# Kernel tuning notes

Measured on AMD Instinct MI355X. Metric: run time of the kernel, lower is better.

## Reference

```python
import jax, jax.numpy as jnp
import numpy as np

VOCAB = 50000
E = 256      # text_embed_dim
K = 512      # num_kernels
KS = 9       # kernel_size
L = 8192     # num labels
B, T = 8, 2048
PAD = KS // 2


def setup_inputs() -> dict:
    key = jax.random.key(0)
    ks = jax.random.split(key, 9)
    ids = jax.random.randint(ks[0], (B, T), 0, VOCAB)
    mask = jnp.ones((B, T), dtype=jnp.int32)  # unused by forward, kept for signature parity
    target = (jax.random.uniform(ks[1], (B, L)) < 0.01).astype(jnp.float32)
    embed_w = jax.random.normal(ks[2], (VOCAB, E), jnp.float32) * 0.02
    conv_w = jax.random.normal(ks[3], (K, E, KS), jnp.float32) * (1.0 / np.sqrt(E * KS))
    conv_b = jnp.zeros((K,), jnp.float32)
    U_w = jax.random.normal(ks[4], (L, K), jnp.float32) * (1.0 / np.sqrt(K))
    final_w = jax.random.normal(ks[5], (L, K), jnp.float32) * (1.0 / np.sqrt(K))
    final_b = jnp.zeros((L,), jnp.float32)
    return {"ids": ids, "mask": mask, "G": 0, "target": target,
            "embed_w": embed_w, "conv_w": conv_w, "conv_b": conv_b,
            "U_w": U_w, "final_w": final_w, "final_b": final_b}


def _forward(ids, embed_w, conv_w, conv_b, U_w, final_w, final_b):
    # embed + (dropout=identity in eval) -> [B, E, T]
    x = embed_w[ids].transpose(0, 2, 1)
    # same-padded Conv1d, then ReLU -> text_feats [B, T, K]
    y = jax.lax.conv_general_dilated(x, conv_w, (1,), [(PAD, PAD)],
                                     dimension_numbers=("NCH", "OIH", "NCH"))
    feats = jax.nn.relu(y + conv_b[None, :, None]).transpose(0, 2, 1)
    # label-wise attention: alpha = softmax(U.weight @ feats^T, dim=2) -> [B, L, T]
    scores = jnp.einsum("lk,btk->blt", U_w, feats)
    alpha = jax.nn.softmax(scores, axis=2)
    # attended features per label -> [B, L, K]
    attn = jnp.einsum("blt,btk->blk", alpha, feats)
    # label-wise dot with final.weight + bias -> logits [B, L]
    yhat = jnp.einsum("blk,lk->bl", attn, final_w) + final_b
    return yhat


def _bce_with_logits(yhat, target):
    # mean over all elements, numerically stable
    return jnp.mean(jnp.maximum(yhat, 0) - yhat * target + jnp.log1p(jnp.exp(-jnp.abs(yhat))))


def reference(ids, mask, G, target, embed_w, conv_w, conv_b, U_w, final_w, final_b):
    yhat = _forward(ids, embed_w, conv_w, conv_b, U_w, final_w, final_b)
    loss = _bce_with_logits(yhat, target)
    return yhat, loss
```

## Files before the change

kernel.cpp:

```cpp
#include <hip/hip_runtime.h>
#include <hip/hip_bf16.h>
#include <cstdint>

#define B_ 8
#define T_ 2048
#define E_ 256
#define K_ 512
#define KS_ 9
#define L_ 8192
#define PAD_ 4
#define TP_ (T_ + 2 * PAD_)
#define KK_ (E_ * KS_)

#define FEAT_SCALE 64.0f
#define W_SCALE 16.0f
#define INV_SS 9.765625e-4f

typedef __bf16 bf16x8 __attribute__((ext_vector_type(8)));
typedef float f32x4 __attribute__((ext_vector_type(4)));
typedef float f32x16 __attribute__((ext_vector_type(16)));
typedef int i32x4 __attribute__((ext_vector_type(4)));
typedef int i32x8 __attribute__((ext_vector_type(8)));

__device__ __forceinline__ unsigned short f2bf(float f) {
  union { float f; unsigned int u; } a; a.f = f;
  unsigned int r = (a.u + 0x7FFFu + ((a.u >> 16) & 1u)) >> 16;
  return (unsigned short)r;
}

__device__ __forceinline__ unsigned char f2fp8(float v) {
  return (unsigned char)(__builtin_amdgcn_cvt_pk_fp8_f32(v, v, 0, false) & 0xFF);
}

__device__ __forceinline__ unsigned int pk4_fp8(float a, float b, float c, float d) {
  int v = __builtin_amdgcn_cvt_pk_fp8_f32(a, b, 0, false);
  v = __builtin_amdgcn_cvt_pk_fp8_f32(c, d, v, true);
  return (unsigned int)v;
}

__device__ __forceinline__ void gld_lds16(const void* g, void* l) {
  __builtin_amdgcn_global_load_lds(
      (const __attribute__((address_space(1))) unsigned int*)g,
      (__attribute__((address_space(3))) unsigned int*)l, 16, 0, 0);
}

__device__ __forceinline__ f32x4 mfma_bf16(bf16x8 a, bf16x8 b, f32x4 c) {
  return __builtin_amdgcn_mfma_f32_16x16x32_bf16(a, b, c, 0, 0, 0);
}

__device__ __forceinline__ f32x16 mfma_sc64(i32x8 a, i32x8 b, f32x16 c) {
  return __builtin_amdgcn_mfma_scale_f32_32x32x64_f8f6f4(a, b, c, 0, 0, 0, 127, 0, 127);
}

__device__ __forceinline__ int swz_off(int k, int row) {
  int ku = k >> 4;
  int slot = ((ku & 7) ^ (row & 7)) | (ku & 24);
  return slot * 16 + (k & 15);
}

__global__ __launch_bounds__(256) void k_embed(const int* __restrict__ ids,
                                               const float* __restrict__ emb,
                                               unsigned short* __restrict__ xpad) {
  int gid = blockIdx.x * 256 + threadIdx.x;
  int row = gid >> 6;
  int e4 = (gid & 63) << 2;
  int b = row / TP_;
  int tp = row - b * TP_;
  float4 v = make_float4(0.f, 0.f, 0.f, 0.f);
  if (tp >= PAD_ && tp < T_ + PAD_) {
    int id = ids[b * T_ + tp - PAD_];
    v = *(const float4*)(emb + (size_t)id * E_ + e4);
  }
  ushort4 o;
  o.x = f2bf(v.x); o.y = f2bf(v.y); o.z = f2bf(v.z); o.w = f2bf(v.w);
  *(ushort4*)(xpad + (size_t)row * E_ + e4) = o;
}

__global__ __launch_bounds__(256) void k_wt(const float* __restrict__ conv_w,
                                            unsigned short* __restrict__ wt) {
  int kk = blockIdx.x * 256 + threadIdx.x;
  int k = blockIdx.y;
  int j = kk >> 8, e = kk & 255;
  wt[(size_t)k * KK_ + kk] = f2bf(conv_w[(k * E_ + e) * KS_ + j]);
}

__global__ __launch_bounds__(256) void k_cast(const float* __restrict__ U_w,
                                              const float* __restrict__ F_w,
                                              unsigned char* __restrict__ u8,
                                              unsigned char* __restrict__ f8) {
  int gid = blockIdx.x * 256 + threadIdx.x;
  const float* src = blockIdx.y ? F_w : U_w;
  unsigned char* dst = blockIdx.y ? f8 : u8;
  int l = gid >> 6;
  int k0 = (gid & 63) << 3;
  const float* s = src + (size_t)l * K_ + k0;
  float4 v0 = *(const float4*)(s);
  float4 v1 = *(const float4*)(s + 4);
  uint2 o;
  o.x = pk4_fp8(v0.x * W_SCALE, v0.y * W_SCALE, v0.z * W_SCALE, v0.w * W_SCALE);
  o.y = pk4_fp8(v1.x * W_SCALE, v1.y * W_SCALE, v1.z * W_SCALE, v1.w * W_SCALE);
  *(uint2*)(dst + (size_t)l * K_ + swz_off(k0, l)) = o;
}

__global__ __launch_bounds__(512, 4) void k_conv(const unsigned short* __restrict__ xpad,
                                                 const unsigned short* __restrict__ wt,
                                                 const float* __restrict__ conv_b,
                                                 unsigned char* __restrict__ feats) {
  __shared__ char At[2][16384];
  __shared__ char Bt[2][16384];
  const int tid = threadIdx.x;
  const int lane = tid & 63;
  const int q = lane >> 4, c = lane & 15;
  const int w = tid >> 6;
  const int wi = w >> 1, wj = w & 1;
  const int b = blockIdx.z;
  const int t0 = blockIdx.y * 128;
  const int n0 = blockIdx.x * 128;

  const char* xb = (const char*)(xpad + (size_t)b * TP_ * E_);
  const char* wb = (const char*)wt;

  const char* asrc[2]; const char* bsrc[2]; int ldso[2];
#pragma unroll
  for (int rnd = 0; rnd < 2; ++rnd) {
    int u = rnd * 512 + tid;
    int r = u >> 3;
    int j = (u & 7) ^ (r & 7);
    asrc[rnd] = xb + (size_t)(t0 + r) * 512 + j * 16;
    bsrc[rnd] = wb + (size_t)(n0 + r) * (KK_ * 2) + j * 16;
    ldso[rnd] = u * 16;
  }

  int offA[2][2], offB[4][2];
#pragma unroll
  for (int li = 0; li < 2; ++li) {
    int r = wi * 32 + li * 16 + c;
#pragma unroll
    for (int h = 0; h < 2; ++h) offA[li][h] = r * 128 + (((4 * h + q) ^ (r & 7)) << 4);
  }
#pragma unroll
  for (int ti = 0; ti < 4; ++ti) {
    int r = wj * 64 + ti * 16 + c;
#pragma unroll
    for (int h = 0; h < 2; ++h) offB[ti][h] = r * 128 + (((4 * h + q) ^ (r & 7)) << 4);
  }

  f32x4 acc[2][4];
  f32x4 zero = {0.f, 0.f, 0.f, 0.f};
#pragma unroll
  for (int i = 0; i < 2; ++i)
#pragma unroll
    for (int j = 0; j < 4; ++j) acc[i][j] = zero;

#pragma unroll
  for (int rnd = 0; rnd < 2; ++rnd) {
    gld_lds16(asrc[rnd], At[0] + ldso[rnd]);
    gld_lds16(bsrc[rnd], Bt[0] + ldso[rnd]);
  }

  for (int it = 0; it < 36; ++it) {
    const int bsel = it & 1;
    __syncthreads();
    if (it != 35) {
      const int kkc = (it + 1) * 64;
      const int aofs = (kkc >> 8) * 512 + (kkc & 255) * 2;
      const int bofs = kkc * 2;
#pragma unroll
      for (int rnd = 0; rnd < 2; ++rnd) {
        gld_lds16(asrc[rnd] + aofs, At[bsel ^ 1] + ldso[rnd]);
        gld_lds16(bsrc[rnd] + bofs, Bt[bsel ^ 1] + ldso[rnd]);
      }
    }
    const char* aB = At[bsel];
    const char* bB = Bt[bsel];
#pragma unroll
    for (int h = 0; h < 2; ++h) {
      bf16x8 afr[2], bfr[4];
#pragma unroll
      for (int li = 0; li < 2; ++li) afr[li] = *(const bf16x8*)(aB + offA[li][h]);
#pragma unroll
      for (int ti = 0; ti < 4; ++ti) bfr[ti] = *(const bf16x8*)(bB + offB[ti][h]);
#pragma unroll
      for (int ti = 0; ti < 4; ++ti)
#pragma unroll
        for (int li = 0; li < 2; ++li)
          acc[li][ti] = mfma_bf16(afr[li], bfr[ti], acc[li][ti]);
    }
  }

#pragma unroll
  for (int ti = 0; ti < 4; ++ti) {
    int k = n0 + wj * 64 + ti * 16 + c;
    float bias = conv_b[k];
#pragma unroll
    for (int li = 0; li < 2; ++li) {
      int tb = t0 + wi * 32 + li * 16 + q * 4;
#pragma unroll
      for (int rr = 0; rr < 4; ++rr) {
        float v = fmaxf(acc[li][ti][rr] + bias, 0.f) * FEAT_SCALE;
        int t = tb + rr;
        feats[(size_t)(b * T_ + t) * K_ + swz_off(k, t)] = f2fp8(v);
      }
    }
  }
}

__global__ __launch_bounds__(512, 2) void k_attn(const unsigned char* __restrict__ feats,
                                                 const unsigned char* __restrict__ u8,
                                                 const unsigned char* __restrict__ f8,
                                                 const float* __restrict__ final_b,
                                                 float* __restrict__ out) {
  __shared__ __align__(16) char smem[131072];
  __shared__ float red[512];
  const int tid = threadIdx.x;
  const int lane = tid & 63;
  const int q2 = lane >> 5, c32 = lane & 31;
  const int w = tid >> 6;
  const int wi = w >> 1;
  const int wj = w & 1;
  const int b = blockIdx.y;
  const int l0 = blockIdx.x * 128;

  const unsigned char* fb = feats + (size_t)b * T_ * K_;

  char* Us = smem;
  char* Ws = smem + 65536;
#pragma unroll
  for (int rr = 0; rr < 8; ++rr) {
    gld_lds16(u8 + (size_t)l0 * K_ + rr * 8192 + tid * 16, Us + rr * 8192 + tid * 16);
    gld_lds16(f8 + (size_t)l0 * K_ + rr * 8192 + tid * 16, Ws + rr * 8192 + tid * 16);
  }
  __syncthreads();

  const int arow = wi * 32 + c32;
  const int ab = arow * 512;
  const int a7 = arow & 7;
  i32x8 uf[8], wf[8];
#pragma unroll
  for (int s = 0; s < 8; ++s) {
    int u0 = s * 4 + q2 * 2;
    int o0 = ab + ((((u0 & 7) ^ a7) | (u0 & 24)) << 4);
    i32x4 ul = *(const i32x4*)(Us + o0);
    i32x4 uh = *(const i32x4*)(Us + (o0 ^ 16));
    i32x4 wl = *(const i32x4*)(Ws + o0);
    i32x4 wh = *(const i32x4*)(Ws + (o0 ^ 16));
    uf[s] = __builtin_shufflevector(ul, uh, 0, 1, 2, 3, 4, 5, 6, 7);
    wf[s] = __builtin_shufflevector(wl, wh, 0, 1, 2, 3, 4, 5, 6, 7);
  }
  __syncthreads();

  char* const Fs0 = smem;
  char* const Fs1 = smem + 32768;
  const unsigned char* fsrc = fb + tid * 16;
#pragma unroll
  for (int rr = 0; rr < 4; ++rr)
    gld_lds16(fsrc + rr * 8192, Fs0 + tid * 16 + rr * 8192);

  const int brow = wj * 32 + c32;
  const int bb = brow * 512;
  const int b7 = brow & 7;
  int foff[8];
#pragma unroll
  for (int s = 0; s < 8; ++s) {
    int u0 = s * 4 + q2 * 2;
    foff[s] = bb + ((((u0 & 7) ^ b7) | (u0 & 24)) << 4);
  }

  f32x16 accS, accV;
  float num[16], den[16];
#pragma unroll
  for (int r = 0; r < 16; ++r) { accS[r] = 0.f; accV[r] = 0.f; num[r] = 0.f; den[r] = 0.f; }

  for (int tc = 0; tc < 32; ++tc) {
    const int bsel = tc & 1;
    char* const cur = bsel ? Fs1 : Fs0;
    char* const nxt = bsel ? Fs0 : Fs1;
    __syncthreads();
    if (tc != 31) {
      const unsigned char* nsrc = fsrc + (tc + 1) * 32768;
#pragma unroll
      for (int rr = 0; rr < 4; ++rr)
        gld_lds16(nsrc + rr * 8192, nxt + tid * 16 + rr * 8192);
    }
#pragma unroll
    for (int s = 0; s < 8; ++s) {
      i32x4 flo = *(const i32x4*)(cur + foff[s]);
      i32x4 fhi = *(const i32x4*)(cur + (foff[s] ^ 16));
      i32x8 fa = __builtin_shufflevector(flo, fhi, 0, 1, 2, 3, 4, 5, 6, 7);
      accS = mfma_sc64(uf[s], fa, accS);
      accV = mfma_sc64(wf[s], fa, accV);
    }
#pragma unroll
    for (int r = 0; r < 16; ++r) {
      float p = __expf(accS[r] * INV_SS);
      den[r] += p;
      num[r] += p * accV[r];
      accS[r] = 0.f;
      accV[r] = 0.f;
    }
  }

#pragma unroll
  for (int r = 0; r < 16; ++r) {
#pragma unroll
    for (int m = 1; m < 32; m <<= 1) {
      num[r] += __shfl_xor(num[r], m, 64);
      den[r] += __shfl_xor(den[r], m, 64);
    }
  }
  if (c32 == 0) {
#pragma unroll
    for (int r = 0; r < 16; ++r) {
      int ll = wi * 32 + (r & 3) + 8 * (r >> 2) + 4 * q2;
      red[wj * 256 + ll] = num[r];
      red[wj * 256 + 128 + ll] = den[r];
    }
  }
  __syncthreads();
  if (tid < 128) {
    int l = l0 + tid;
    float n = red[tid] + red[256 + tid];
    float d = red[128 + tid] + red[384 + tid];
    out[(size_t)b * L_ + l] = (n * INV_SS) / d + final_b[l];
  }
}

__global__ __launch_bounds__(256) void k_loss(const float* __restrict__ yhat,
                                              const float* __restrict__ target,
                                              float* __restrict__ loss) {
  int gid = blockIdx.x * 256 + threadIdx.x;
  float s = 0.f;
  for (int i = gid; i < B_ * L_; i += 64 * 256) {
    float y = yhat[i], t = target[i];
    s += fmaxf(y, 0.f) - y * t + log1pf(__expf(-fabsf(y)));
  }
#pragma unroll
  for (int m = 1; m < 64; m <<= 1) s += __shfl_xor(s, m, 64);
  if ((threadIdx.x & 63) == 0) atomicAdd(loss, s * (1.0f / (B_ * L_)));
}

extern "C" void kernel_launch(void* const* d_in, const int* in_sizes, int n_in,
                              void* d_out, int out_size, void* d_ws, size_t ws_size,
                              hipStream_t stream) {
  const int* ids = (const int*)d_in[0];
  const float* target = (const float*)d_in[3];
  const float* emb = (const float*)d_in[4];
  const float* conv_w = (const float*)d_in[5];
  const float* conv_b = (const float*)d_in[6];
  const float* U_w = (const float*)d_in[7];
  const float* F_w = (const float*)d_in[8];
  const float* final_b = (const float*)d_in[9];
  float* out = (float*)d_out;

  char* ws = (char*)d_ws;
  unsigned short* xpad = (unsigned short*)ws;
  size_t off = (size_t)B_ * TP_ * E_ * 2;
  unsigned short* wt = (unsigned short*)(ws + off);
  off += (size_t)K_ * KK_ * 2;
  unsigned char* u8 = (unsigned char*)(ws + off);
  off += (size_t)L_ * K_;
  unsigned char* f8 = (unsigned char*)(ws + off);
  off += (size_t)L_ * K_;
  unsigned char* feats = (unsigned char*)(ws + off);
  off += (size_t)B_ * T_ * K_;
  if (ws_size < off) return;

  k_embed<<<dim3((B_ * TP_ * 64) / 256), 256, 0, stream>>>(ids, emb, xpad);
  k_wt<<<dim3(KK_ / 256, K_), 256, 0, stream>>>(conv_w, wt);
  k_cast<<<dim3((L_ * K_ / 8) / 256, 2), 256, 0, stream>>>(U_w, F_w, u8, f8);
  k_conv<<<dim3(K_ / 128, T_ / 128, B_), 512, 0, stream>>>(xpad, wt, conv_b, feats);
  k_attn<<<dim3(L_ / 128, B_), 512, 0, stream>>>(feats, u8, f8, final_b, out);
  hipMemsetAsync(out + B_ * L_, 0, sizeof(float), stream);
  k_loss<<<dim3(64), 256, 0, stream>>>(out, target, out + B_ * L_);
}
```

Baseline: 288.0 us.

## Store feats and fp8 weights in k-chunk-major tiles, use exp2 in softmax

Replaces the XOR-swizzled row-major layout of the fp8 features and weight matrices with a blocked layout: 16-byte k-chunks are stored contiguously across rows within each 64-row (feats) or 128-row (weights) tile. LDS fragment reads in the attention kernel then become simple constant-offset loads without per-iteration swizzle arithmetic, and consecutive lanes read consecutive 16-byte chunks, which is meant to avoid bank conflicts. The exponential is computed with exp2 and a pre-folded log2(e) scale. The conv epilogue now writes scattered single bytes into the new layout, which may cost more on the store side.

New measurement: 295.6 us. 1.03x slower.

```diff
diff --git a/kernel.cpp b/kernel.cpp
--- a/kernel.cpp
+++ b/kernel.cpp
@@ -15,6 +15,7 @@
 #define FEAT_SCALE 64.0f
 #define W_SCALE 16.0f
 #define INV_SS 9.765625e-4f
+#define INV_SS_LOG2E 1.40888719e-3f
 
 typedef __bf16 bf16x8 __attribute__((ext_vector_type(8)));
 typedef float f32x4 __attribute__((ext_vector_type(4)));
@@ -52,10 +53,11 @@
   return __builtin_amdgcn_mfma_scale_f32_32x32x64_f8f6f4(a, b, c, 0, 0, 0, 127, 0, 127);
 }
 
-__device__ __forceinline__ int swz_off(int k, int row) {
-  int ku = k >> 4;
-  int slot = ((ku & 7) ^ (row & 7)) | (ku & 24);
-  return slot * 16 + (k & 15);
+__device__ __forceinline__ int f_off(int t, int k) {
+  return ((t >> 6) * 32768) + (((k >> 4) * 64 + (t & 63)) << 4) + (k & 15);
+}
+__device__ __forceinline__ int w_off(int l, int k) {
+  return ((l >> 7) * 65536) + (((k >> 4) * 128 + (l & 127)) << 4) + (k & 15);
 }
 
 __global__ __launch_bounds__(256) void k_embed(const int* __restrict__ ids,
@@ -99,7 +101,7 @@
   uint2 o;
   o.x = pk4_fp8(v0.x * W_SCALE, v0.y * W_SCALE, v0.z * W_SCALE, v0.w * W_SCALE);
   o.y = pk4_fp8(v1.x * W_SCALE, v1.y * W_SCALE, v1.z * W_SCALE, v1.w * W_SCALE);
-  *(uint2*)(dst + (size_t)l * K_ + swz_off(k0, l)) = o;
+  *(uint2*)(dst + w_off(l, k0)) = o;
 }
 
 __global__ __launch_bounds__(512, 4) void k_conv(const unsigned short* __restrict__ xpad,
@@ -188,6 +190,7 @@
     }
   }
 
+  const size_t fbase = (size_t)b * T_ * K_;
 #pragma unroll
   for (int ti = 0; ti < 4; ++ti) {
     int k = n0 + wj * 64 + ti * 16 + c;
@@ -199,7 +202,7 @@
       for (int rr = 0; rr < 4; ++rr) {
         float v = fmaxf(acc[li][ti][rr] + bias, 0.f) * FEAT_SCALE;
         int t = tb + rr;
-        feats[(size_t)(b * T_ + t) * K_ + swz_off(k, t)] = f2fp8(v);
+        feats[fbase + f_off(t, k)] = f2fp8(v);
       }
     }
   }
@@ -233,17 +236,15 @@
   __syncthreads();
 
   const int arow = wi * 32 + c32;
-  const int ab = arow * 512;
-  const int a7 = arow & 7;
+  const int abase = q2 * 4096 + arow * 16;
   i32x8 uf[8], wf[8];
 #pragma unroll
   for (int s = 0; s < 8; ++s) {
-    int u0 = s * 4 + q2 * 2;
-    int o0 = ab + ((((u0 & 7) ^ a7) | (u0 & 24)) << 4);
+    int o0 = abase + s * 8192;
     i32x4 ul = *(const i32x4*)(Us + o0);
-    i32x4 uh = *(const i32x4*)(Us + (o0 ^ 16));
+    i32x4 uh = *(const i32x4*)(Us + o0 + 2048);
     i32x4 wl = *(const i32x4*)(Ws + o0);
-    i32x4 wh = *(const i32x4*)(Ws + (o0 ^ 16));
+    i32x4 wh = *(const i32x4*)(Ws + o0 + 2048);
     uf[s] = __builtin_shufflevector(ul, uh, 0, 1, 2, 3, 4, 5, 6, 7);
     wf[s] = __builtin_shufflevector(wl, wh, 0, 1, 2, 3, 4, 5, 6, 7);
   }
@@ -257,14 +258,7 @@
     gld_lds16(fsrc + rr * 8192, Fs0 + tid * 16 + rr * 8192);
 
   const int brow = wj * 32 + c32;
-  const int bb = brow * 512;
-  const int b7 = brow & 7;
-  int foff[8];
-#pragma unroll
-  for (int s = 0; s < 8; ++s) {
-    int u0 = s * 4 + q2 * 2;
-    foff[s] = bb + ((((u0 & 7) ^ b7) | (u0 & 24)) << 4);
-  }
+  const int bbase = q2 * 2048 + brow * 16;
 
   f32x16 accS, accV;
   float num[16], den[16];
@@ -284,15 +278,15 @@
     }
 #pragma unroll
     for (int s = 0; s < 8; ++s) {
-      i32x4 flo = *(const i32x4*)(cur + foff[s]);
-      i32x4 fhi = *(const i32x4*)(cur + (foff[s] ^ 16));
+      i32x4 flo = *(const i32x4*)(cur + bbase + s * 4096);
+      i32x4 fhi = *(const i32x4*)(cur + bbase + s * 4096 + 1024);
       i32x8 fa = __builtin_shufflevector(flo, fhi, 0, 1, 2, 3, 4, 5, 6, 7);
       accS = mfma_sc64(uf[s], fa, accS);
       accV = mfma_sc64(wf[s], fa, accV);
     }
 #pragma unroll
     for (int r = 0; r < 16; ++r) {
-      float p = __expf(accS[r] * INV_SS);
+      float p = __builtin_exp2f(accS[r] * INV_SS_LOG2E);
       den[r] += p;
       num[r] += p * accV[r];
       accS[r] = 0.f;
```
